# Kernel tuning notes

Hardware: AMD Instinct MI355X
Metric: run time of the kernel (lower is better)

Reference implementation:

```python
import jax, jax.numpy as jnp
import numpy as np

N_INPUTS = 1024
MAX_HIDDEN_PER_LAYER = 2048
MAX_LAYERS = 4
TOTAL_HIDDEN = MAX_HIDDEN_PER_LAYER * MAX_LAYERS
N_OUTPUTS = 512
MAX_CONNECTIONS = 2048
MAX_OUTPUT_CONNECTIONS = 4096


def setup_inputs() -> dict:
    key = jax.random.key(0)
    ks = jax.random.split(key, 4)
    return {
        "input_values": jax.random.normal(ks[0], (N_INPUTS,), dtype=jnp.float32),
        "hidden_incoming_ids": jax.random.randint(ks[1], (TOTAL_HIDDEN, MAX_CONNECTIONS), 0, N_INPUTS + TOTAL_HIDDEN, dtype=jnp.int32),
        "hidden_weights": jax.random.normal(ks[2], (TOTAL_HIDDEN, MAX_CONNECTIONS), dtype=jnp.float32) * (1.0 / np.sqrt(MAX_CONNECTIONS)),
        "hidden_conn_mask": jnp.ones((TOTAL_HIDDEN, MAX_CONNECTIONS), dtype=bool),
        "hidden_active_mask": jnp.ones((TOTAL_HIDDEN,), dtype=bool),
        "output_incoming_ids": jax.random.randint(ks[3], (N_OUTPUTS, MAX_OUTPUT_CONNECTIONS), 0, N_INPUTS + TOTAL_HIDDEN, dtype=jnp.int32),
        "output_weights": jax.random.normal(jax.random.fold_in(key, 7), (N_OUTPUTS, MAX_OUTPUT_CONNECTIONS), dtype=jnp.float32) * (1.0 / np.sqrt(MAX_OUTPUT_CONNECTIONS)),
        "output_conn_mask": jnp.ones((N_OUTPUTS, MAX_OUTPUT_CONNECTIONS), dtype=bool),
    }


def reference(input_values, hidden_incoming_ids, hidden_weights, hidden_conn_mask,
              hidden_active_mask, output_incoming_ids, output_weights, output_conn_mask):
    # values vector over all source neurons: [n_inputs + total_hidden]
    values = jnp.concatenate([input_values, jnp.zeros((TOTAL_HIDDEN,), dtype=input_values.dtype)])
    # sequential layer-by-layer forward (layer_boundaries semantics)
    for k in range(MAX_LAYERS):
        start = k * MAX_HIDDEN_PER_LAYER
        end = start + MAX_HIDDEN_PER_LAYER
        ids = hidden_incoming_ids[start:end]          # [H, C]
        w = hidden_weights[start:end]                 # [H, C]
        cmask = hidden_conn_mask[start:end]           # [H, C]
        amask = hidden_active_mask[start:end]         # [H]
        gathered = values[ids]                        # irregular gather [H, C]
        pre = jnp.sum(gathered * w * cmask, axis=-1)  # weighted sum per neuron
        act = jnp.tanh(pre) * amask                   # forward_fn = tanh, inactive -> 0
        values = values.at[N_INPUTS + start:N_INPUTS + end].set(act)
    # output neurons: gather + weighted sum, linear output_forward_fn
    g_out = values[output_incoming_ids]               # [O, Co]
    outputs = jnp.sum(g_out * output_weights * output_conn_mask, axis=-1)
    return outputs
```

## Files before the change

### kernel.cpp

```cpp
#include <hip/hip_runtime.h>

#define N_INPUTS   1024
#define MAX_HIDDEN 2048
#define MAX_LAYERS 4
#define TOTAL_HIDDEN 8192
#define N_OUTPUTS  512
#define MAX_CONN   2048
#define MAX_OUT_CONN 4096
#define N_VALUES   9216

__device__ __forceinline__ void stage_values(float* __restrict__ vals,
                                             const float* __restrict__ g_in,
                                             const float* __restrict__ gvals,
                                             int staged_hidden)
{
    const float4* in4 = reinterpret_cast<const float4*>(g_in);
    const float4* gv4 = reinterpret_cast<const float4*>(gvals);
    float4* s4 = reinterpret_cast<float4*>(vals);
    const int nin4 = N_INPUTS >> 2;
    const int pre4 = (N_INPUTS + staged_hidden) >> 2;
    for (int i = threadIdx.x; i < (N_VALUES >> 2); i += blockDim.x) {
        float4 v;
        if (i < nin4)      v = in4[i];
        else if (i < pre4) v = gv4[i - nin4];
        else { v.x = 0.f; v.y = 0.f; v.z = 0.f; v.w = 0.f; }
        s4[i] = v;
    }
}

__device__ __forceinline__ float dot4(int4 ia, float4 wa, int4 ma,
                                      const float* __restrict__ vals)
{
    float s = 0.f;
    s = fmaf(ma.x ? vals[ia.x] : 0.f, wa.x, s);
    s = fmaf(ma.y ? vals[ia.y] : 0.f, wa.y, s);
    s = fmaf(ma.z ? vals[ia.z] : 0.f, wa.z, s);
    s = fmaf(ma.w ? vals[ia.w] : 0.f, wa.w, s);
    return s;
}

__global__ void __launch_bounds__(1024, 8)
hidden_layer_kernel(const float* __restrict__ g_in,
                    float* __restrict__ gvals,
                    const int* __restrict__ ids,
                    const float* __restrict__ wts,
                    const int* __restrict__ cmask,
                    const int* __restrict__ amask,
                    int row_base)
{
    __shared__ float vals[N_VALUES];
    __shared__ float psum[16];

    const int tid  = threadIdx.x;
    const int wave = tid >> 6;
    const int lane = tid & 63;

    const int neuron = (blockIdx.x << 2) + (wave >> 2);
    const int q      = wave & 3;
    const size_t c0  = (size_t)(row_base + neuron) * MAX_CONN + (q << 9) + (lane << 2);

    int4   ia0 = *reinterpret_cast<const int4*>(ids + c0);
    float4 wa0 = *reinterpret_cast<const float4*>(wts + c0);
    int4   ma0 = *reinterpret_cast<const int4*>(cmask + c0);
    int4   ia1 = *reinterpret_cast<const int4*>(ids + c0 + 256);
    float4 wa1 = *reinterpret_cast<const float4*>(wts + c0 + 256);
    int4   ma1 = *reinterpret_cast<const int4*>(cmask + c0 + 256);

    stage_values(vals, g_in, gvals, row_base);
    __syncthreads();

    float sum = dot4(ia0, wa0, ma0, vals) + dot4(ia1, wa1, ma1, vals);

    #pragma unroll
    for (int off = 32; off > 0; off >>= 1)
        sum += __shfl_xor(sum, off, 64);

    if (lane == 0) psum[wave] = sum;
    __syncthreads();

    if (tid < 4) {
        const int n = (blockIdx.x << 2) + tid;
        float s = psum[(tid << 2)] + psum[(tid << 2) + 1]
                + psum[(tid << 2) + 2] + psum[(tid << 2) + 3];
        float a = tanhf(s);
        if (amask[row_base + n] == 0) a = 0.f;
        gvals[row_base + n] = a;
    }
}

__global__ void __launch_bounds__(1024, 8)
output_layer_kernel(const float* __restrict__ g_in,
                    const float* __restrict__ gvals,
                    const int* __restrict__ ids,
                    const float* __restrict__ wts,
                    const int* __restrict__ cmask,
                    float* __restrict__ out)
{
    __shared__ float vals[N_VALUES];
    __shared__ float psum[16];

    const int tid  = threadIdx.x;
    const int wave = tid >> 6;
    const int lane = tid & 63;

    const size_t c0 = (size_t)blockIdx.x * MAX_OUT_CONN + (wave << 8) + (lane << 2);

    int4   ia = *reinterpret_cast<const int4*>(ids + c0);
    float4 wa = *reinterpret_cast<const float4*>(wts + c0);
    int4   ma = *reinterpret_cast<const int4*>(cmask + c0);

    stage_values(vals, g_in, gvals, TOTAL_HIDDEN);
    __syncthreads();

    float sum = dot4(ia, wa, ma, vals);

    #pragma unroll
    for (int off = 32; off > 0; off >>= 1)
        sum += __shfl_xor(sum, off, 64);

    if (lane == 0) psum[wave] = sum;
    __syncthreads();

    if (tid == 0) {
        float s = 0.f;
        #pragma unroll
        for (int q = 0; q < 16; ++q) s += psum[q];
        out[blockIdx.x] = s;
    }
}

extern "C" void kernel_launch(void* const* d_in, const int* in_sizes, int n_in,
                              void* d_out, int out_size, void* d_ws, size_t ws_size,
                              hipStream_t stream) {
    const float* input_values = (const float*)d_in[0];
    const int*   h_ids        = (const int*)d_in[1];
    const float* h_w          = (const float*)d_in[2];
    const int*   h_cm         = (const int*)d_in[3];
    const int*   h_am         = (const int*)d_in[4];
    const int*   o_ids        = (const int*)d_in[5];
    const float* o_w          = (const float*)d_in[6];
    const int*   o_cm         = (const int*)d_in[7];
    float* out   = (float*)d_out;
    float* gvals = (float*)d_ws;

    for (int k = 0; k < MAX_LAYERS; ++k) {
        hidden_layer_kernel<<<512, 1024, 0, stream>>>(
            input_values, gvals, h_ids, h_w, h_cm, h_am, k * MAX_HIDDEN);
    }

    output_layer_kernel<<<512, 1024, 0, stream>>>(
        input_values, gvals, o_ids, o_w, o_cm, out);
}
```

Measured before the change: 51.31 us.

## Fuse all layers into one cooperative persistent kernel with grid barriers

```diff
diff --git a/kernel.cpp b/kernel.cpp
--- a/kernel.cpp
+++ b/kernel.cpp
@@ -8,6 +8,152 @@
 #define MAX_CONN   2048
 #define MAX_OUT_CONN 4096
 #define N_VALUES   9216
+#define FB 256
+#define FT 1024
+
+typedef int   v4i __attribute__((ext_vector_type(4)));
+typedef float v4f __attribute__((ext_vector_type(4)));
+
+struct G { v4i ia; v4f wa; v4i ma; };
+
+__device__ __forceinline__ void load_g(G& g,
+        const int* __restrict__ ids, const float* __restrict__ wts,
+        const int* __restrict__ cm, size_t c)
+{
+    g.ia = *reinterpret_cast<const v4i*>(ids + c);
+    g.wa = *reinterpret_cast<const v4f*>(wts + c);
+    g.ma = *reinterpret_cast<const v4i*>(cm + c);
+}
+
+__device__ __forceinline__ float dot_g(const G& g, const float* __restrict__ vals)
+{
+    float s = 0.f;
+    s = fmaf(g.ma.x ? vals[g.ia.x] : 0.f, g.wa.x, s);
+    s = fmaf(g.ma.y ? vals[g.ia.y] : 0.f, g.wa.y, s);
+    s = fmaf(g.ma.z ? vals[g.ia.z] : 0.f, g.wa.z, s);
+    s = fmaf(g.ma.w ? vals[g.ia.w] : 0.f, g.wa.w, s);
+    return s;
+}
+
+#define KEEP_G(g) asm volatile("" : "+v"((g).ia), "+v"((g).wa), "+v"((g).ma))
+
+__global__ void init_bar_kernel(unsigned* __restrict__ bar) {
+    if (threadIdx.x < MAX_LAYERS) bar[threadIdx.x * 32] = 0u;
+}
+
+__global__ void __launch_bounds__(FT, 4)
+fused_net(const float* __restrict__ g_in,
+          const int* __restrict__ h_ids, const float* __restrict__ h_w,
+          const int* __restrict__ h_cm,  const int* __restrict__ h_am,
+          const int* __restrict__ o_ids, const float* __restrict__ o_w,
+          const int* __restrict__ o_cm,
+          float* __restrict__ out, float* __restrict__ gvals,
+          unsigned* __restrict__ bar)
+{
+    __shared__ float vals[N_VALUES];
+    __shared__ float psum[16];
+
+    const int tid  = threadIdx.x;
+    const int wave = tid >> 6;
+    const int lane = tid & 63;
+
+    const size_t LSTRIDE = (size_t)MAX_HIDDEN * MAX_CONN;
+    const size_t hbase = ((size_t)(blockIdx.x << 3) + (wave >> 1)) * MAX_CONN
+                       + ((size_t)(wave & 1) << 10) + (lane << 2);
+    const size_t obase = ((size_t)(blockIdx.x << 1) + (wave >> 3)) * MAX_OUT_CONN
+                       + ((size_t)(wave & 7) << 9) + (lane << 2);
+
+    G cur[4], nxt[4];
+
+    #pragma unroll
+    for (int j = 0; j < 4; ++j)
+        load_g(cur[j], h_ids, h_w, h_cm, hbase + (size_t)(j << 8));
+    KEEP_G(cur[0]); KEEP_G(cur[1]); KEEP_G(cur[2]); KEEP_G(cur[3]);
+
+    {
+        const v4f* in4 = reinterpret_cast<const v4f*>(g_in);
+        v4f* s4 = reinterpret_cast<v4f*>(vals);
+        for (int i = tid; i < (N_VALUES >> 2); i += FT) {
+            v4f v;
+            if (i < (N_INPUTS >> 2)) v = in4[i];
+            else { v.x = 0.f; v.y = 0.f; v.z = 0.f; v.w = 0.f; }
+            s4[i] = v;
+        }
+    }
+    __syncthreads();
+
+    #pragma unroll
+    for (int k = 0; k < MAX_LAYERS; ++k) {
+        float sum = 0.f;
+        #pragma unroll
+        for (int j = 0; j < 4; ++j) sum += dot_g(cur[j], vals);
+
+        #pragma unroll
+        for (int off = 32; off > 0; off >>= 1)
+            sum += __shfl_xor(sum, off, 64);
+
+        if (lane == 0) psum[wave] = sum;
+        __syncthreads();
+
+        if (tid < 8) {
+            const int n = k * MAX_HIDDEN + (blockIdx.x << 3) + tid;
+            float s = psum[tid << 1] + psum[(tid << 1) + 1];
+            float a = tanhf(s);
+            if (h_am[n] == 0) a = 0.f;
+            (void)__hip_atomic_exchange(&gvals[n], a, __ATOMIC_RELAXED,
+                                        __HIP_MEMORY_SCOPE_AGENT);
+        }
+
+        if (k < MAX_LAYERS - 1) {
+            #pragma unroll
+            for (int j = 0; j < 4; ++j)
+                load_g(nxt[j], h_ids, h_w, h_cm,
+                       (size_t)(k + 1) * LSTRIDE + hbase + (size_t)(j << 8));
+            KEEP_G(nxt[0]); KEEP_G(nxt[1]); KEEP_G(nxt[2]); KEEP_G(nxt[3]);
+        } else {
+            load_g(nxt[0], o_ids, o_w, o_cm, obase);
+            load_g(nxt[1], o_ids, o_w, o_cm, obase + 256);
+            KEEP_G(nxt[0]); KEEP_G(nxt[1]);
+        }
+
+        __syncthreads();
+        if (tid == 0) {
+            __builtin_amdgcn_s_waitcnt(0);
+            asm volatile("" ::: "memory");
+            __hip_atomic_fetch_add(&bar[k * 32], 1u, __ATOMIC_RELAXED,
+                                   __HIP_MEMORY_SCOPE_AGENT);
+            while (__hip_atomic_load(&bar[k * 32], __ATOMIC_RELAXED,
+                                     __HIP_MEMORY_SCOPE_AGENT) != FB)
+                __builtin_amdgcn_s_sleep(2);
+            asm volatile("" ::: "memory");
+        }
+        __syncthreads();
+
+        for (int i = tid; i < MAX_HIDDEN; i += FT)
+            vals[N_INPUTS + k * MAX_HIDDEN + i] =
+                __hip_atomic_load(&gvals[k * MAX_HIDDEN + i], __ATOMIC_RELAXED,
+                                  __HIP_MEMORY_SCOPE_AGENT);
+        __syncthreads();
+
+        #pragma unroll
+        for (int j = 0; j < 4; ++j) cur[j] = nxt[j];
+    }
+
+    {
+        float sum = dot_g(cur[0], vals) + dot_g(cur[1], vals);
+        #pragma unroll
+        for (int off = 32; off > 0; off >>= 1)
+            sum += __shfl_xor(sum, off, 64);
+        if (lane == 0) psum[wave] = sum;
+        __syncthreads();
+        if (tid < 2) {
+            float s = 0.f;
+            #pragma unroll
+            for (int q = 0; q < 8; ++q) s += psum[(tid << 3) + q];
+            out[(blockIdx.x << 1) + tid] = s;
+        }
+    }
+}
 
 __device__ __forceinline__ void stage_values(float* __restrict__ vals,
                                              const float* __restrict__ g_in,
@@ -140,14 +286,25 @@
     const int*   o_ids        = (const int*)d_in[5];
     const float* o_w          = (const float*)d_in[6];
     const int*   o_cm         = (const int*)d_in[7];
-    float* out   = (float*)d_out;
-    float* gvals = (float*)d_ws;
-
-    for (int k = 0; k < MAX_LAYERS; ++k) {
-        hidden_layer_kernel<<<512, 1024, 0, stream>>>(
-            input_values, gvals, h_ids, h_w, h_cm, h_am, k * MAX_HIDDEN);
-    }
-
-    output_layer_kernel<<<512, 1024, 0, stream>>>(
-        input_values, gvals, o_ids, o_w, o_cm, out);
-}
+    float*    out   = (float*)d_out;
+    float*    gvals = (float*)d_ws;
+    unsigned* bar   = (unsigned*)(gvals + TOTAL_HIDDEN);
+
+    int nb = 0;
+    (void)hipOccupancyMaxActiveBlocksPerMultiprocessor(&nb, fused_net, FT, 0);
+
+    if (nb >= 1) {
+        init_bar_kernel<<<1, 64, 0, stream>>>(bar);
+        void* args[] = { (void*)&input_values, (void*)&h_ids, (void*)&h_w, (void*)&h_cm,
+                         (void*)&h_am, (void*)&o_ids, (void*)&o_w, (void*)&o_cm,
+                         (void*)&out, (void*)&gvals, (void*)&bar };
+        hipLaunchCooperativeKernel((const void*)fused_net, dim3(FB), dim3(FT),
+                                   args, 0, stream);
+    } else {
+        for (int k = 0; k < MAX_LAYERS; ++k)
+            hidden_layer_kernel<<<512, 1024, 0, stream>>>(
+                input_values, gvals, h_ids, h_w, h_cm, h_am, k * MAX_HIDDEN);
+        output_layer_kernel<<<512, 1024, 0, stream>>>(
+            input_values, gvals, o_ids, o_w, o_cm, out);
+    }
+}
```

Measured after the change: 51.48 us. No clear change (+0.3%).

## Stage only computed values and halve block size in layer kernels

Applied to the files above, without the earlier changes.

```diff
diff --git a/kernel.cpp b/kernel.cpp
--- a/kernel.cpp
+++ b/kernel.cpp
@@ -9,23 +9,15 @@
 #define MAX_OUT_CONN 4096
 #define N_VALUES   9216
 
-__device__ __forceinline__ void stage_values(float* __restrict__ vals,
-                                             const float* __restrict__ g_in,
-                                             const float* __restrict__ gvals,
-                                             int staged_hidden)
+__device__ __forceinline__ float dot4b(int4 ia, float4 wa, int4 ma,
+                                       const float* __restrict__ vals, int bound)
 {
-    const float4* in4 = reinterpret_cast<const float4*>(g_in);
-    const float4* gv4 = reinterpret_cast<const float4*>(gvals);
-    float4* s4 = reinterpret_cast<float4*>(vals);
-    const int nin4 = N_INPUTS >> 2;
-    const int pre4 = (N_INPUTS + staged_hidden) >> 2;
-    for (int i = threadIdx.x; i < (N_VALUES >> 2); i += blockDim.x) {
-        float4 v;
-        if (i < nin4)      v = in4[i];
-        else if (i < pre4) v = gv4[i - nin4];
-        else { v.x = 0.f; v.y = 0.f; v.z = 0.f; v.w = 0.f; }
-        s4[i] = v;
-    }
+    float s = 0.f;
+    s = fmaf((ma.x && ia.x < bound) ? vals[ia.x] : 0.f, wa.x, s);
+    s = fmaf((ma.y && ia.y < bound) ? vals[ia.y] : 0.f, wa.y, s);
+    s = fmaf((ma.z && ia.z < bound) ? vals[ia.z] : 0.f, wa.z, s);
+    s = fmaf((ma.w && ia.w < bound) ? vals[ia.w] : 0.f, wa.w, s);
+    return s;
 }
 
 __device__ __forceinline__ float dot4(int4 ia, float4 wa, int4 ma,
@@ -39,7 +31,7 @@
     return s;
 }
 
-__global__ void __launch_bounds__(1024, 8)
+__global__ void __launch_bounds__(512, 8)
 hidden_layer_kernel(const float* __restrict__ g_in,
                     float* __restrict__ gvals,
                     const int* __restrict__ ids,
@@ -49,13 +41,13 @@
                     int row_base)
 {
     __shared__ float vals[N_VALUES];
-    __shared__ float psum[16];
+    __shared__ float psum[8];
 
     const int tid  = threadIdx.x;
     const int wave = tid >> 6;
     const int lane = tid & 63;
 
-    const int neuron = (blockIdx.x << 2) + (wave >> 2);
+    const int neuron = (blockIdx.x << 1) + (wave >> 2);
     const int q      = wave & 3;
     const size_t c0  = (size_t)(row_base + neuron) * MAX_CONN + (q << 9) + (lane << 2);
 
@@ -66,7 +58,70 @@
     float4 wa1 = *reinterpret_cast<const float4*>(wts + c0 + 256);
     int4   ma1 = *reinterpret_cast<const int4*>(cmask + c0 + 256);
 
-    stage_values(vals, g_in, gvals, row_base);
+    const int bound = N_INPUTS + row_base;
+    {
+        const float4* in4 = reinterpret_cast<const float4*>(g_in);
+        const float4* gv4 = reinterpret_cast<const float4*>(gvals);
+        float4* s4 = reinterpret_cast<float4*>(vals);
+        const int nin4 = N_INPUTS >> 2;
+        const int pre4 = bound >> 2;
+        for (int i = tid; i < pre4; i += 512)
+            s4[i] = (i < nin4) ? in4[i] : gv4[i - nin4];
+    }
+    __syncthreads();
+
+    float sum = dot4b(ia0, wa0, ma0, vals, bound)
+              + dot4b(ia1, wa1, ma1, vals, bound);
+
+    #pragma unroll
+    for (int off = 32; off > 0; off >>= 1)
+        sum += __shfl_xor(sum, off, 64);
+
+    if (lane == 0) psum[wave] = sum;
+    __syncthreads();
+
+    if (tid < 2) {
+        const int n = (blockIdx.x << 1) + tid;
+        float s = psum[(tid << 2)] + psum[(tid << 2) + 1]
+                + psum[(tid << 2) + 2] + psum[(tid << 2) + 3];
+        float a = tanhf(s);
+        if (amask[row_base + n] == 0) a = 0.f;
+        gvals[row_base + n] = a;
+    }
+}
+
+__global__ void __launch_bounds__(512, 8)
+output_layer_kernel(const float* __restrict__ g_in,
+                    const float* __restrict__ gvals,
+                    const int* __restrict__ ids,
+                    const float* __restrict__ wts,
+                    const int* __restrict__ cmask,
+                    float* __restrict__ out)
+{
+    __shared__ float vals[N_VALUES];
+    __shared__ float psum[8];
+
+    const int tid  = threadIdx.x;
+    const int wave = tid >> 6;
+    const int lane = tid & 63;
+
+    const size_t c0 = (size_t)blockIdx.x * MAX_OUT_CONN + (wave << 9) + (lane << 2);
+
+    int4   ia0 = *reinterpret_cast<const int4*>(ids + c0);
+    float4 wa0 = *reinterpret_cast<const float4*>(wts + c0);
+    int4   ma0 = *reinterpret_cast<const int4*>(cmask + c0);
+    int4   ia1 = *reinterpret_cast<const int4*>(ids + c0 + 256);
+    float4 wa1 = *reinterpret_cast<const float4*>(wts + c0 + 256);
+    int4   ma1 = *reinterpret_cast<const int4*>(cmask + c0 + 256);
+
+    {
+        const float4* in4 = reinterpret_cast<const float4*>(g_in);
+        const float4* gv4 = reinterpret_cast<const float4*>(gvals);
+        float4* s4 = reinterpret_cast<float4*>(vals);
+        const int nin4 = N_INPUTS >> 2;
+        for (int i = tid; i < (N_VALUES >> 2); i += 512)
+            s4[i] = (i < nin4) ? in4[i] : gv4[i - nin4];
+    }
     __syncthreads();
 
     float sum = dot4(ia0, wa0, ma0, vals) + dot4(ia1, wa1, ma1, vals);
@@ -78,53 +133,10 @@
     if (lane == 0) psum[wave] = sum;
     __syncthreads();
 
-    if (tid < 4) {
-        const int n = (blockIdx.x << 2) + tid;
-        float s = psum[(tid << 2)] + psum[(tid << 2) + 1]
-                + psum[(tid << 2) + 2] + psum[(tid << 2) + 3];
-        float a = tanhf(s);
-        if (amask[row_base + n] == 0) a = 0.f;
-        gvals[row_base + n] = a;
-    }
-}
-
-__global__ void __launch_bounds__(1024, 8)
-output_layer_kernel(const float* __restrict__ g_in,
-                    const float* __restrict__ gvals,
-                    const int* __restrict__ ids,
-                    const float* __restrict__ wts,
-                    const int* __restrict__ cmask,
-                    float* __restrict__ out)
-{
-    __shared__ float vals[N_VALUES];
-    __shared__ float psum[16];
-
-    const int tid  = threadIdx.x;
-    const int wave = tid >> 6;
-    const int lane = tid & 63;
-
-    const size_t c0 = (size_t)blockIdx.x * MAX_OUT_CONN + (wave << 8) + (lane << 2);
-
-    int4   ia = *reinterpret_cast<const int4*>(ids + c0);
-    float4 wa = *reinterpret_cast<const float4*>(wts + c0);
-    int4   ma = *reinterpret_cast<const int4*>(cmask + c0);
-
-    stage_values(vals, g_in, gvals, TOTAL_HIDDEN);
-    __syncthreads();
-
-    float sum = dot4(ia, wa, ma, vals);
-
-    #pragma unroll
-    for (int off = 32; off > 0; off >>= 1)
-        sum += __shfl_xor(sum, off, 64);
-
-    if (lane == 0) psum[wave] = sum;
-    __syncthreads();
-
     if (tid == 0) {
         float s = 0.f;
         #pragma unroll
-        for (int q = 0; q < 16; ++q) s += psum[q];
+        for (int q = 0; q < 8; ++q) s += psum[q];
         out[blockIdx.x] = s;
     }
 }
@@ -144,10 +156,10 @@
     float* gvals = (float*)d_ws;
 
     for (int k = 0; k < MAX_LAYERS; ++k) {
-        hidden_layer_kernel<<<512, 1024, 0, stream>>>(
+        hidden_layer_kernel<<<1024, 512, 0, stream>>>(
             input_values, gvals, h_ids, h_w, h_cm, h_am, k * MAX_HIDDEN);
     }
 
-    output_layer_kernel<<<512, 1024, 0, stream>>>(
+    output_layer_kernel<<<512, 512, 0, stream>>>(
         input_values, gvals, o_ids, o_w, o_cm, out);
 }
```

Result: faster. 48.18 us (median of 2 runs) (-6.1%).
